# Kernel optimization log

Measured on AMD Instinct MI355X. Metric: run time of the kernel, lower is better.

Reference implementation:

```python
import jax, jax.numpy as jnp
import numpy as np

V, D, H, F, L, M, T, B, MAXT = 32000, 1024, 16, 4096, 3, 1, 1024, 2, 2048
HD = D // H

def _ln(x, g, b, eps=1e-5):
    m = x.mean(-1, keepdims=True)
    v = ((x - m) ** 2).mean(-1, keepdims=True)
    return (x - m) * jax.lax.rsqrt(v + eps) * g + b

def _mha(x, Wq, bq, Wk, bk, Wv, bv, Wo, bo, mask):
    Bx, Tx, Dx = x.shape
    q = (x @ Wq.T + bq).reshape(Bx, Tx, H, HD)
    k = (x @ Wk.T + bk).reshape(Bx, Tx, H, HD)
    v = (x @ Wv.T + bv).reshape(Bx, Tx, H, HD)
    s = jnp.einsum('bqhd,bkhd->bhqk', q, k) / np.float32(np.sqrt(HD))
    s = jnp.where(mask[None, None], s, jnp.float32(-1e9))
    a = jax.nn.softmax(s, axis=-1)
    o = jnp.einsum('bhqk,bkhd->bqhd', a, v).reshape(Bx, Tx, Dx)
    return o @ Wo.T + bo

def setup_inputs() -> dict:
    key = jax.random.key(0)
    ks = iter(jax.random.split(key, 64))
    rn = lambda shape: jax.random.normal(next(ks), shape, jnp.float32) * 0.02
    inp = {
        'x': jax.random.randint(next(ks), (B, T), 0, V),
        'mask': jnp.tril(jnp.ones((T, T), bool)),  # causal mask
        'tok_W': rn((V, D)),  # embedding table = Linear(V,D).weight.T
        'pos_embed': rn((MAXT, D)),
        'Wq': rn((L, D, D)), 'bq': jnp.zeros((L, D)),
        'Wk': rn((L, D, D)), 'bk': jnp.zeros((L, D)),
        'Wv': rn((L, D, D)), 'bv': jnp.zeros((L, D)),
        'Wo': rn((L, D, D)), 'bo': jnp.zeros((L, D)),
        'ln1_g': jnp.ones((L, D)), 'ln1_b': jnp.zeros((L, D)),
        'W1': rn((L, F, D)), 'b1': jnp.zeros((L, F)),
        'W2': rn((L, D, F)), 'b2': jnp.zeros((L, D)),
        'ln2_g': jnp.ones((L, D)), 'ln2_b': jnp.zeros((L, D)),
        'mWq': rn((M, D, D)), 'mbq': jnp.zeros((M, D)),
        'mWk': rn((M, D, D)), 'mbk': jnp.zeros((M, D)),
        'mWv': rn((M, D, D)), 'mbv': jnp.zeros((M, D)),
        'mWo': rn((M, D, D)), 'mbo': jnp.zeros((M, D)),
        'mln_g': jnp.ones((M, D)), 'mln_b': jnp.zeros((M, D)),
        'tWq': rn((D, D)), 'tbq': jnp.zeros((D,)),
        'tWk': rn((D, D)), 'tbk': jnp.zeros((D,)),
        'tWv': rn((D, D)), 'tbv': jnp.zeros((D,)),
        'tWo': rn((D, D)), 'tbo': jnp.zeros((D,)),
        'tln_g': jnp.ones((D,)), 'tln_b': jnp.zeros((D,)),
        'norm_g': jnp.ones((D,)), 'norm_b': jnp.zeros((D,)),
        'out_W': rn((V, D)), 'out_b': jnp.zeros((V,)),
    }
    return inp

def reference(x, mask, tok_W, pos_embed, Wq, bq, Wk, bk, Wv, bv, Wo, bo,
              ln1_g, ln1_b, W1, b1, W2, b2, ln2_g, ln2_b,
              mWq, mbq, mWk, mbk, mWv, mbv, mWo, mbo, mln_g, mln_b,
              tWq, tbq, tWk, tbk, tWv, tbv, tWo, tbo, tln_g, tln_b,
              norm_g, norm_b, out_W, out_b):
    Bx, Tx = x.shape
    # one_hot(x, V).float() @ W_tok^T  ==  gather row x from the (V, D) table
    h = jnp.take(tok_W, x, axis=0) + pos_embed[:Tx][None]
    mi = 0
    for i in range(L):  # static small layer count
        a = _mha(h, Wq[i], bq[i], Wk[i], bk[i], Wv[i], bv[i], Wo[i], bo[i], mask)
        h = _ln(h + a, ln1_g[i], ln1_b[i])
        f = jax.nn.gelu(h @ W1[i].T + b1[i]) @ W2[i].T + b2[i]
        h = _ln(h + f, ln2_g[i], ln2_b[i])
        if i % 3 == 2 and mi < M:  # memory layer every 3rd block
            a = _mha(h, mWq[mi], mbq[mi], mWk[mi], mbk[mi], mWv[mi], mbv[mi], mWo[mi], mbo[mi], mask)
            h = _ln(h + a, mln_g[mi], mln_b[mi])
            mi += 1
    a = _mha(h, tWq, tbq, tWk, tbk, tWv, tbv, tWo, tbo, mask)  # thought attention
    h = _ln(h + a, tln_g, tln_b)
    h = _ln(h, norm_g, norm_b)
    return h @ out_W.T + out_b  # [B, T, V] logits
```

## Files before the change

kernel.cpp:

```cpp
#include <hip/hip_runtime.h>
#include <cstdint>

#define DEV static __device__ __forceinline__

typedef unsigned short u16;
typedef __attribute__((ext_vector_type(8))) short short8;
typedef __attribute__((ext_vector_type(4))) float f32x4;

namespace cfg {
constexpr int V = 32000, D = 1024, H = 16, F = 4096, L = 3, T = 1024, B = 2;
constexpr int N = B * T;
constexpr int HD = D / H;
}

DEV float bf2f(u16 b) { union { unsigned u; float f; } x; x.u = (unsigned)b << 16; return x.f; }
DEV u16 f2bf(float f) {
  union { float f; unsigned u; } x; x.f = f;
  unsigned u = x.u;
  return (u16)((u + 0x7fffu + ((u >> 16) & 1u)) >> 16);
}

DEV void gload16(void* lds, const void* g) {
  __builtin_amdgcn_global_load_lds((__attribute__((address_space(1))) void*)g,
                                   (__attribute__((address_space(3))) void*)lds, 16, 0, 0);
}

DEV float waveSum(float v) {
#pragma unroll
  for (int o = 32; o; o >>= 1) v += __shfl_xor(v, o);
  return v;
}

struct CastJob { const float* src; u16* dst; int nBlk; };
struct CastArgs { CastJob j[24]; int n; };

__global__ void cast_kernel(CastArgs a) {
  int blk = blockIdx.x;
  int i = 0;
  while (i + 1 < a.n && blk >= a.j[i].nBlk) { blk -= a.j[i].nBlk; ++i; }
  const size_t base = (size_t)blk * 2048 + threadIdx.x * 8;
  const float4* s4 = (const float4*)(a.j[i].src + base);
  const float4 v0 = s4[0], v1 = s4[1];
  short8 o;
  o[0] = (short)f2bf(v0.x); o[1] = (short)f2bf(v0.y);
  o[2] = (short)f2bf(v0.z); o[3] = (short)f2bf(v0.w);
  o[4] = (short)f2bf(v1.x); o[5] = (short)f2bf(v1.y);
  o[6] = (short)f2bf(v1.z); o[7] = (short)f2bf(v1.w);
  *(short8*)(a.j[i].dst + base) = o;
}

struct CopyJob { const float* src; float* dst; };
struct CopyArgs { CopyJob j[16]; int n; };
__global__ void bconcat_kernel(CopyArgs a) {
  const CopyJob jb = a.j[blockIdx.x];
  ((float4*)jb.dst)[threadIdx.x] = ((const float4*)jb.src)[threadIdx.x];
}

__global__ void embed_kernel(const int* __restrict__ x, const float* __restrict__ tokW,
                             const float* __restrict__ pos, float* __restrict__ hF,
                             u16* __restrict__ hB) {
  const int bt = blockIdx.x;
  const int t = bt & (cfg::T - 1);
  const int tid = threadIdx.x;
  const int idx = x[bt];
  float4 v = ((const float4*)(tokW + (size_t)idx * cfg::D))[tid];
  const float4 p = ((const float4*)(pos + (size_t)t * cfg::D))[tid];
  v.x += p.x; v.y += p.y; v.z += p.z; v.w += p.w;
  ((float4*)(hF + (size_t)bt * cfg::D))[tid] = v;
  union { u16 u[4]; uint2 q; } pk;
  pk.u[0] = f2bf(v.x); pk.u[1] = f2bf(v.y); pk.u[2] = f2bf(v.z); pk.u[3] = f2bf(v.w);
  *(uint2*)(hB + (size_t)bt * cfg::D + tid * 4) = pk.q;
}

__global__ void ln_kernel(const float* __restrict__ base, const float* __restrict__ add,
                          const float* __restrict__ g, const float* __restrict__ bt,
                          float* __restrict__ outF, u16* __restrict__ outB) {
  const int row = blockIdx.x, tid = threadIdx.x;
  const int lane = tid & 63, wid = tid >> 6;
  float4 x = ((const float4*)(base + (size_t)row * cfg::D))[tid];
  if (add) {
    const float4 a = ((const float4*)(add + (size_t)row * cfg::D))[tid];
    x.x += a.x; x.y += a.y; x.z += a.z; x.w += a.w;
  }
  float s = x.x + x.y + x.z + x.w;
  float s2 = x.x * x.x + x.y * x.y + x.z * x.z + x.w * x.w;
  __shared__ float sb[8];
  s = waveSum(s); s2 = waveSum(s2);
  if (lane == 0) { sb[wid] = s; sb[4 + wid] = s2; }
  __syncthreads();
  s = sb[0] + sb[1] + sb[2] + sb[3];
  s2 = sb[4] + sb[5] + sb[6] + sb[7];
  const float mean = s * (1.f / cfg::D);
  const float rs = rsqrtf(s2 * (1.f / cfg::D) - mean * mean + 1e-5f);
  const float4 gv = ((const float4*)g)[tid];
  const float4 bv = ((const float4*)bt)[tid];
  float4 y;
  y.x = (x.x - mean) * rs * gv.x + bv.x;
  y.y = (x.y - mean) * rs * gv.y + bv.y;
  y.z = (x.z - mean) * rs * gv.z + bv.z;
  y.w = (x.w - mean) * rs * gv.w + bv.w;
  ((float4*)(outF + (size_t)row * cfg::D))[tid] = y;
  union { u16 u[4]; uint2 q; } pk;
  pk.u[0] = f2bf(y.x); pk.u[1] = f2bf(y.y); pk.u[2] = f2bf(y.z); pk.u[3] = f2bf(y.w);
  *(uint2*)(outB + (size_t)row * cfg::D + tid * 4) = pk.q;
}

__global__ void vtrans_kernel(const u16* __restrict__ v, u16* __restrict__ vtO, int vstride) {
  __shared__ u16 s[64][68];
  const int bh = blockIdx.y, b = bh >> 4, h = bh & 15;
  const int t0 = blockIdx.x * 64;
  const int tid = threadIdx.x;
  const int r2 = tid >> 3, cg = tid & 7;
#pragma unroll
  for (int p = 0; p < 2; ++p) {
    const int r = p * 32 + r2;
    const short8 val = *(const short8*)(v + (size_t)(b * cfg::T + t0 + r) * vstride + h * 64 + cg * 8);
#pragma unroll
    for (int j = 0; j < 8; ++j) s[r][cg * 8 + j] = (u16)val[j];
  }
  __syncthreads();
#pragma unroll
  for (int p = 0; p < 2; ++p) {
    const int d = p * 32 + r2;
    short8 o;
#pragma unroll
    for (int j = 0; j < 8; ++j) o[j] = (short)s[cg * 8 + j][d];
    *(short8*)(vtO + ((size_t)bh * 64 + d) * (size_t)cfg::T + t0 + cg * 8) = o;
  }
}

template <int NCH>
DEV void stageTile(u16* lds, const u16* src, int strideElems, int tid) {
#pragma unroll
  for (int c = 0; c < NCH / 256; ++c) {
    const int ci = c * 256 + tid;
    const int r = ci >> 3;
    const int c8 = ci & 7;
    const int sc8 = c8 ^ (r & 7);
    gload16(lds + (size_t)ci * 8, src + (size_t)r * strideElems + sc8 * 8);
  }
}
DEV short8 ldsFrag(const u16* tile, int row, int kElem) {
  const int byteoff = row * 128 + ((kElem * 2) ^ ((row & 7) << 4));
  return *(const short8*)((const char*)tile + byteoff);
}

__launch_bounds__(256, 2)
__global__ void fattn_kernel(const u16* __restrict__ qkv, const u16* __restrict__ vt,
                             u16* __restrict__ o) {
  constexpr int D3 = 3 * cfg::D;
  __shared__ u16 Qs[64 * 64];
  __shared__ u16 Ks[64 * 64];
  __shared__ u16 Vs[64 * 64];
  __shared__ u16 Ps[64][72];
  const int tid = threadIdx.x, lane = tid & 63, w = tid >> 6;
  const int qt = blockIdx.x, bh = blockIdx.y;
  const int b = bh >> 4, h = bh & 15;
  const int q0 = qt * 64;
  const int l15 = lane & 15, lq = lane >> 4;

  stageTile<512>(Qs, qkv + (size_t)(b * cfg::T + q0) * D3 + h * 64, D3, tid);
  __syncthreads();
  short8 qf[2];
#pragma unroll
  for (int kk = 0; kk < 2; ++kk)
    qf[kk] = ldsFrag(Qs, w * 16 + l15, kk * 32 + lq * 8);

  f32x4 oa[4];
  float m[4], l[4];
#pragma unroll
  for (int r = 0; r < 4; ++r) { m[r] = -1e30f; l[r] = 0.f; }
#pragma unroll
  for (int nt = 0; nt < 4; ++nt) { oa[nt][0] = 0; oa[nt][1] = 0; oa[nt][2] = 0; oa[nt][3] = 0; }

  const int nkt = qt + 1;
  const u16* kbase = qkv + (size_t)(b * cfg::T) * D3 + cfg::D + h * 64;
  const u16* vbase = vt + (size_t)bh * 64 * cfg::T;

  for (int kt = 0; kt < nkt; ++kt) {
    const int k0 = kt * 64;
    __syncthreads();
    stageTile<512>(Ks, kbase + (size_t)k0 * D3, D3, tid);
    stageTile<512>(Vs, vbase + k0, cfg::T, tid);
    __syncthreads();

    f32x4 sa[4];
#pragma unroll
    for (int nt = 0; nt < 4; ++nt) { sa[nt][0] = 0; sa[nt][1] = 0; sa[nt][2] = 0; sa[nt][3] = 0; }
#pragma unroll
    for (int kk = 0; kk < 2; ++kk) {
      short8 kf[4];
#pragma unroll
      for (int nt = 0; nt < 4; ++nt) kf[nt] = ldsFrag(Ks, nt * 16 + l15, kk * 32 + lq * 8);
#pragma unroll
      for (int nt = 0; nt < 4; ++nt)
        sa[nt] = __builtin_amdgcn_mfma_f32_16x16x32_bf16(qf[kk], kf[nt], sa[nt], 0, 0, 0);
    }

    const bool needMask = (kt >= qt);
#pragma unroll
    for (int r = 0; r < 4; ++r) {
      const int qrow = q0 + w * 16 + lq * 4 + r;
      float s[4];
#pragma unroll
      for (int nt = 0; nt < 4; ++nt) {
        s[nt] = sa[nt][r] * 0.125f;
        if (needMask && (k0 + nt * 16 + l15 > qrow)) s[nt] = -3e38f;
      }
      float rm = fmaxf(fmaxf(s[0], s[1]), fmaxf(s[2], s[3]));
#pragma unroll
      for (int off = 1; off < 16; off <<= 1) rm = fmaxf(rm, __shfl_xor(rm, off));
      const float mn = fmaxf(m[r], rm);
      const float sc = __expf(m[r] - mn);
      m[r] = mn;
      float ps = 0.f;
#pragma unroll
      for (int nt = 0; nt < 4; ++nt) {
        const float p = __expf(s[nt] - mn);
        ps += p;
        Ps[w * 16 + lq * 4 + r][nt * 16 + l15] = f2bf(p);
      }
#pragma unroll
      for (int off = 1; off < 16; off <<= 1) ps += __shfl_xor(ps, off);
      l[r] = l[r] * sc + ps;
#pragma unroll
      for (int nt = 0; nt < 4; ++nt) oa[nt][r] *= sc;
    }

#pragma unroll
    for (int kk = 0; kk < 2; ++kk) {
      short8 pa = *(const short8*)&Ps[w * 16 + l15][kk * 32 + lq * 8];
      short8 vf[4];
#pragma unroll
      for (int nt = 0; nt < 4; ++nt) vf[nt] = ldsFrag(Vs, nt * 16 + l15, kk * 32 + lq * 8);
#pragma unroll
      for (int nt = 0; nt < 4; ++nt)
        oa[nt] = __builtin_amdgcn_mfma_f32_16x16x32_bf16(pa, vf[nt], oa[nt], 0, 0, 0);
    }
  }

  u16* obase = o + (size_t)(b * cfg::T + q0 + w * 16) * cfg::D + h * 64;
#pragma unroll
  for (int r = 0; r < 4; ++r) {
    const float inv = 1.f / l[r];
    const int rl = lq * 4 + r;
#pragma unroll
    for (int nt = 0; nt < 4; ++nt)
      obase[(size_t)rl * cfg::D + nt * 16 + l15] = f2bf(oa[nt][r] * inv);
  }
}

template <int BN, int EPI, int OUTF32, int SWZ, int MMAJOR>
__launch_bounds__(256, 4)
__global__ void gemm_kernel(const u16* __restrict__ A, const u16* __restrict__ Bw,
                            const float* __restrict__ bias, void* __restrict__ Cp,
                            int lda, int ldb, int ldc, int K) {
  constexpr int BM = 128, BK = 64;
  constexpr int WN = BN / 2;
  constexpr int MF = 4, NF = WN / 16;
  int bx = blockIdx.x, by = blockIdx.y;
  if (SWZ) {
    const int gx = gridDim.x;
    const int nwg = gx * gridDim.y;
    const int lid = by * gx + bx;
    const int q = nwg >> 3, r = nwg & 7;
    const int xcd = lid & 7, rest = lid >> 3;
    const int nid = (xcd < r ? xcd * (q + 1) : r * (q + 1) + (xcd - r) * q) + rest;
    bx = nid % gx; by = nid / gx;
  }
  const int tid = threadIdx.x;
  const int lane = tid & 63;
  const int wid = tid >> 6;
  const int wr = wid >> 1, wc = wid & 1;
  const int m0 = (MMAJOR ? bx : by) * BM;
  const int n0 = (MMAJOR ? by : bx) * BN;

  __shared__ u16 As[BM][BK];
  __shared__ u16 Bs[BN][BK];

  const int nkt = K / BK;

  f32x4 acc[MF][NF];
#pragma unroll
  for (int i = 0; i < MF; ++i)
#pragma unroll
    for (int j = 0; j < NF; ++j) {
      acc[i][j][0] = 0.f; acc[i][j][1] = 0.f; acc[i][j][2] = 0.f; acc[i][j][3] = 0.f;
    }

  for (int kt = 0; kt < nkt; ++kt) {
    __syncthreads();
    const int kb = kt * BK;
    stageTile<(BM * BK) / 8>(&As[0][0], A + (size_t)m0 * lda + kb, lda, tid);
    stageTile<(BN * BK) / 8>(&Bs[0][0], Bw + (size_t)n0 * ldb + kb, ldb, tid);
    __syncthreads();
#pragma unroll
    for (int kk = 0; kk < BK / 32; ++kk) {
      short8 av[MF], bv[NF];
      const int kElem = kk * 32 + (lane >> 4) * 8;
#pragma unroll
      for (int mt = 0; mt < MF; ++mt)
        av[mt] = ldsFrag(&As[0][0], wr * 64 + mt * 16 + (lane & 15), kElem);
#pragma unroll
      for (int nt = 0; nt < NF; ++nt)
        bv[nt] = ldsFrag(&Bs[0][0], wc * WN + nt * 16 + (lane & 15), kElem);
#pragma unroll
      for (int mt = 0; mt < MF; ++mt)
#pragma unroll
        for (int nt = 0; nt < NF; ++nt)
          acc[mt][nt] = __builtin_amdgcn_mfma_f32_16x16x32_bf16(av[mt], bv[nt], acc[mt][nt], 0, 0, 0);
    }
  }

  const int rhi = (lane >> 4) * 4, cidx = lane & 15;
#pragma unroll
  for (int mt = 0; mt < MF; ++mt) {
#pragma unroll
    for (int nt = 0; nt < NF; ++nt) {
      const int col = n0 + wc * WN + nt * 16 + cidx;
      const float badd = bias ? bias[col] : 0.f;
#pragma unroll
      for (int r = 0; r < 4; ++r) {
        const int row = m0 + wr * 64 + mt * 16 + rhi + r;
        float val = acc[mt][nt][r] + badd;
        if (EPI == 1) {
          const float zz = 1.5957691216057308f * (val + 0.044715f * val * val * val);
          const float th = 1.f - 2.f / (__expf(zz) + 1.f);
          val = 0.5f * val * (1.f + th);
        }
        const size_t off = (size_t)row * ldc + col;
        if (OUTF32) ((float*)Cp)[off] = val;
        else ((u16*)Cp)[off] = f2bf(val);
      }
    }
  }
}

extern "C" void kernel_launch(void* const* d_in, const int* in_sizes, int n_in,
                              void* d_out, int out_size, void* d_ws, size_t ws_size,
                              hipStream_t stream) {
  using namespace cfg;
  (void)in_sizes; (void)n_in; (void)out_size;
  const int* x = (const int*)d_in[0];
  const float* tokW = (const float*)d_in[2];
  const float* pos = (const float*)d_in[3];
  const float* Wq = (const float*)d_in[4];  const float* bq = (const float*)d_in[5];
  const float* Wk = (const float*)d_in[6];  const float* bk = (const float*)d_in[7];
  const float* Wv = (const float*)d_in[8];  const float* bv = (const float*)d_in[9];
  const float* Wo = (const float*)d_in[10]; const float* bo = (const float*)d_in[11];
  const float* ln1g = (const float*)d_in[12]; const float* ln1b = (const float*)d_in[13];
  const float* W1 = (const float*)d_in[14]; const float* b1 = (const float*)d_in[15];
  const float* W2 = (const float*)d_in[16]; const float* b2 = (const float*)d_in[17];
  const float* ln2g = (const float*)d_in[18]; const float* ln2b = (const float*)d_in[19];
  const float* mWq = (const float*)d_in[20]; const float* mbq = (const float*)d_in[21];
  const float* mWk = (const float*)d_in[22]; const float* mbk = (const float*)d_in[23];
  const float* mWv = (const float*)d_in[24]; const float* mbv = (const float*)d_in[25];
  const float* mWo = (const float*)d_in[26]; const float* mbo = (const float*)d_in[27];
  const float* mlng = (const float*)d_in[28]; const float* mlnb = (const float*)d_in[29];
  const float* tWq = (const float*)d_in[30]; const float* tbq = (const float*)d_in[31];
  const float* tWk = (const float*)d_in[32]; const float* tbk = (const float*)d_in[33];
  const float* tWv = (const float*)d_in[34]; const float* tbv = (const float*)d_in[35];
  const float* tWo = (const float*)d_in[36]; const float* tbo = (const float*)d_in[37];
  const float* tlng = (const float*)d_in[38]; const float* tlnb = (const float*)d_in[39];
  const float* normg = (const float*)d_in[40]; const float* normb = (const float*)d_in[41];
  const float* outW = (const float*)d_in[42]; const float* outb = (const float*)d_in[43];

  const size_t DD = (size_t)D * D;
  char* wsb = (char*)d_ws;
  size_t off = 0;
  auto alloc = [&](size_t bytes) {
    void* p = wsb + off;
    off += (bytes + 255) & ~(size_t)255;
    return p;
  };
  u16* qkvW = (u16*)alloc((size_t)L * 3 * DD * 2);
  u16* mqkvW = (u16*)alloc(3 * DD * 2);
  u16* tqkvW = (u16*)alloc(3 * DD * 2);
  u16* WoB = (u16*)alloc((size_t)L * DD * 2);
  u16* W1B = (u16*)alloc((size_t)L * F * D * 2);
  u16* W2B = (u16*)alloc((size_t)L * D * F * 2);
  u16* mWoB = (u16*)alloc(DD * 2);
  u16* tWoB = (u16*)alloc(DD * 2);
  u16* outWB = (u16*)alloc((size_t)V * D * 2);
  float* biasQKV = (float*)alloc((size_t)(L + 2) * 3 * D * 4);
  float* hF = (float*)alloc((size_t)N * D * 4);
  u16* hB = (u16*)alloc((size_t)N * D * 2);
  float* aF = (float*)alloc((size_t)N * D * 4);
  u16* qkvB = (u16*)alloc((size_t)N * 3 * D * 2);
  u16* vtB = (u16*)alloc((size_t)N * D * 2);
  u16* oB = (u16*)alloc((size_t)N * D * 2);
  u16* f1B = (u16*)alloc((size_t)N * F * 2);
  if (off > ws_size) return;

  CastArgs ca;
  int nj = 0; long total = 0;
  auto addJob = [&](const float* s, u16* dptr, size_t n) {
    ca.j[nj].src = s; ca.j[nj].dst = dptr; ca.j[nj].nBlk = (int)(n / 2048);
    total += (long)(n / 2048); ++nj;
  };
  for (int i = 0; i < L; ++i) {
    addJob(Wq + i * DD, qkvW + (size_t)i * 3 * DD, DD);
    addJob(Wk + i * DD, qkvW + (size_t)i * 3 * DD + DD, DD);
    addJob(Wv + i * DD, qkvW + (size_t)i * 3 * DD + 2 * DD, DD);
  }
  addJob(mWq, mqkvW, DD); addJob(mWk, mqkvW + DD, DD); addJob(mWv, mqkvW + 2 * DD, DD);
  addJob(tWq, tqkvW, DD); addJob(tWk, tqkvW + DD, DD); addJob(tWv, tqkvW + 2 * DD, DD);
  addJob(Wo, WoB, (size_t)L * DD);
  addJob(W1, W1B, (size_t)L * F * D);
  addJob(W2, W2B, (size_t)L * D * F);
  addJob(mWo, mWoB, DD); addJob(tWo, tWoB, DD);
  addJob(outW, outWB, (size_t)V * D);
  ca.n = nj;
  cast_kernel<<<dim3((unsigned)total), 256, 0, stream>>>(ca);

  CopyArgs cpa;
  int nc = 0;
  auto addCopy = [&](const float* s, float* dptr) { cpa.j[nc].src = s; cpa.j[nc].dst = dptr; ++nc; };
  for (int i = 0; i < L; ++i) {
    addCopy(bq + (size_t)i * D, biasQKV + (size_t)i * 3 * D);
    addCopy(bk + (size_t)i * D, biasQKV + (size_t)i * 3 * D + D);
    addCopy(bv + (size_t)i * D, biasQKV + (size_t)i * 3 * D + 2 * D);
  }
  addCopy(mbq, biasQKV + (size_t)L * 3 * D); addCopy(mbk, biasQKV + (size_t)L * 3 * D + D);
  addCopy(mbv, biasQKV + (size_t)L * 3 * D + 2 * D);
  addCopy(tbq, biasQKV + (size_t)(L + 1) * 3 * D); addCopy(tbk, biasQKV + (size_t)(L + 1) * 3 * D + D);
  addCopy(tbv, biasQKV + (size_t)(L + 1) * 3 * D + 2 * D);
  cpa.n = nc;
  bconcat_kernel<<<dim3((unsigned)nc), 256, 0, stream>>>(cpa);

  embed_kernel<<<N, 256, 0, stream>>>(x, tokW, pos, hF, hB);

  auto mha = [&](const u16* qkvw, const float* qkvbias, const u16* wo, const float* bo_) {
    gemm_kernel<64, 0, 0, 0, 0><<<dim3(3 * D / 64, N / 128, 1), 256, 0, stream>>>(
        hB, qkvw, qkvbias, qkvB, D, D, 3 * D, D);
    vtrans_kernel<<<dim3(T / 64, B * H), 256, 0, stream>>>(qkvB + 2 * D, vtB, 3 * D);
    fattn_kernel<<<dim3(T / 64, B * H), 256, 0, stream>>>(qkvB, vtB, oB);
    gemm_kernel<64, 0, 1, 0, 0><<<dim3(D / 64, N / 128, 1), 256, 0, stream>>>(
        oB, wo, bo_, aF, D, D, D, D);
  };

  auto lnK = [&](const float* addp, const float* g, const float* b_) {
    ln_kernel<<<N, 256, 0, stream>>>(hF, addp, g, b_, hF, hB);
  };

  int mi = 0;
  for (int i = 0; i < L; ++i) {
    mha(qkvW + (size_t)i * 3 * DD, biasQKV + (size_t)i * 3 * D,
        WoB + (size_t)i * DD, bo + (size_t)i * D);
    lnK(aF, ln1g + (size_t)i * D, ln1b + (size_t)i * D);
    gemm_kernel<64, 1, 0, 0, 0><<<dim3(F / 64, N / 128, 1), 256, 0, stream>>>(
        hB, W1B + (size_t)i * F * D, b1 + (size_t)i * F, f1B, D, D, F, D);
    gemm_kernel<64, 0, 1, 0, 0><<<dim3(D / 64, N / 128, 1), 256, 0, stream>>>(
        f1B, W2B + (size_t)i * D * F, b2 + (size_t)i * D, aF, F, F, D, F);
    lnK(aF, ln2g + (size_t)i * D, ln2b + (size_t)i * D);
    if (i % 3 == 2 && mi < 1) {
      mha(mqkvW, biasQKV + (size_t)L * 3 * D, mWoB, mbo);
      lnK(aF, mlng, mlnb);
      ++mi;
    }
  }
  mha(tqkvW, biasQKV + (size_t)(L + 1) * 3 * D, tWoB, tbo);
  lnK(aF, tlng, tlnb);
  lnK(nullptr, normg, normb);
  gemm_kernel<128, 0, 1, 1, 1><<<dim3(N / 128, V / 128, 1), 256, 0, stream>>>(
      hB, outWB, outb, (float*)d_out, D, D, V, D);
}
```

Before: 1.059 ms.

## Split-K the Wo and W2 GEMMs and reduce partials inside layernorm

Measured after the change: 940.2 us. 11.2% less time.

```diff
diff --git a/kernel.cpp b/kernel.cpp
--- a/kernel.cpp
+++ b/kernel.cpp
@@ -72,14 +72,35 @@
   *(uint2*)(hB + (size_t)bt * cfg::D + tid * 4) = pk.q;
 }
 
-__global__ void ln_kernel(const float* __restrict__ base, const float* __restrict__ add,
+template <int NADD>
+__global__ void ln_kernel(const float* __restrict__ base,
+                          const float* __restrict__ a0, const float* __restrict__ a1,
+                          const float* __restrict__ a2, const float* __restrict__ a3,
+                          const float* __restrict__ biasv,
                           const float* __restrict__ g, const float* __restrict__ bt,
                           float* __restrict__ outF, u16* __restrict__ outB) {
   const int row = blockIdx.x, tid = threadIdx.x;
   const int lane = tid & 63, wid = tid >> 6;
-  float4 x = ((const float4*)(base + (size_t)row * cfg::D))[tid];
-  if (add) {
-    const float4 a = ((const float4*)(add + (size_t)row * cfg::D))[tid];
+  const size_t roff = (size_t)row * cfg::D;
+  float4 x = ((const float4*)(base + roff))[tid];
+  if (NADD >= 1) {
+    const float4 a = ((const float4*)(a0 + roff))[tid];
+    x.x += a.x; x.y += a.y; x.z += a.z; x.w += a.w;
+  }
+  if (NADD >= 2) {
+    const float4 a = ((const float4*)(a1 + roff))[tid];
+    x.x += a.x; x.y += a.y; x.z += a.z; x.w += a.w;
+  }
+  if (NADD >= 3) {
+    const float4 a = ((const float4*)(a2 + roff))[tid];
+    x.x += a.x; x.y += a.y; x.z += a.z; x.w += a.w;
+  }
+  if (NADD >= 4) {
+    const float4 a = ((const float4*)(a3 + roff))[tid];
+    x.x += a.x; x.y += a.y; x.z += a.z; x.w += a.w;
+  }
+  if (biasv) {
+    const float4 a = ((const float4*)biasv)[tid];
     x.x += a.x; x.y += a.y; x.z += a.z; x.w += a.w;
   }
   float s = x.x + x.y + x.z + x.w;
@@ -99,10 +120,10 @@
   y.y = (x.y - mean) * rs * gv.y + bv.y;
   y.z = (x.z - mean) * rs * gv.z + bv.z;
   y.w = (x.w - mean) * rs * gv.w + bv.w;
-  ((float4*)(outF + (size_t)row * cfg::D))[tid] = y;
+  ((float4*)(outF + roff))[tid] = y;
   union { u16 u[4]; uint2 q; } pk;
   pk.u[0] = f2bf(y.x); pk.u[1] = f2bf(y.y); pk.u[2] = f2bf(y.z); pk.u[3] = f2bf(y.w);
-  *(uint2*)(outB + (size_t)row * cfg::D + tid * 4) = pk.q;
+  *(uint2*)(outB + roff + tid * 4) = pk.q;
 }
 
 __global__ void vtrans_kernel(const u16* __restrict__ v, u16* __restrict__ vtO, int vstride) {
@@ -254,7 +275,7 @@
 __launch_bounds__(256, 4)
 __global__ void gemm_kernel(const u16* __restrict__ A, const u16* __restrict__ Bw,
                             const float* __restrict__ bias, void* __restrict__ Cp,
-                            int lda, int ldb, int ldc, int K) {
+                            int lda, int ldb, int ldc, int K, long long partStride) {
   constexpr int BM = 128, BK = 64;
   constexpr int WN = BN / 2;
   constexpr int MF = 4, NF = WN / 16;
@@ -268,6 +289,9 @@
     const int nid = (xcd < r ? xcd * (q + 1) : r * (q + 1) + (xcd - r) * q) + rest;
     bx = nid % gx; by = nid / gx;
   }
+  const int z = blockIdx.z;
+  const u16* Ab = A + (size_t)z * K;
+  const u16* Bb = Bw + (size_t)z * K;
   const int tid = threadIdx.x;
   const int lane = tid & 63;
   const int wid = tid >> 6;
@@ -291,8 +315,8 @@
   for (int kt = 0; kt < nkt; ++kt) {
     __syncthreads();
     const int kb = kt * BK;
-    stageTile<(BM * BK) / 8>(&As[0][0], A + (size_t)m0 * lda + kb, lda, tid);
-    stageTile<(BN * BK) / 8>(&Bs[0][0], Bw + (size_t)n0 * ldb + kb, ldb, tid);
+    stageTile<(BM * BK) / 8>(&As[0][0], Ab + (size_t)m0 * lda + kb, lda, tid);
+    stageTile<(BN * BK) / 8>(&Bs[0][0], Bb + (size_t)n0 * ldb + kb, ldb, tid);
     __syncthreads();
 #pragma unroll
     for (int kk = 0; kk < BK / 32; ++kk) {
@@ -313,6 +337,7 @@
   }
 
   const int rhi = (lane >> 4) * 4, cidx = lane & 15;
+  const long long cb = (long long)z * partStride;
 #pragma unroll
   for (int mt = 0; mt < MF; ++mt) {
 #pragma unroll
@@ -328,7 +353,7 @@
           const float th = 1.f - 2.f / (__expf(zz) + 1.f);
           val = 0.5f * val * (1.f + th);
         }
-        const size_t off = (size_t)row * ldc + col;
+        const size_t off = (size_t)(cb + (long long)row * ldc + col);
         if (OUTF32) ((float*)Cp)[off] = val;
         else ((u16*)Cp)[off] = f2bf(val);
       }
@@ -366,6 +391,7 @@
   const float* outW = (const float*)d_in[42]; const float* outb = (const float*)d_in[43];
 
   const size_t DD = (size_t)D * D;
+  const long long ND = (long long)N * D;
   char* wsb = (char*)d_ws;
   size_t off = 0;
   auto alloc = [&](size_t bytes) {
@@ -385,7 +411,7 @@
   float* biasQKV = (float*)alloc((size_t)(L + 2) * 3 * D * 4);
   float* hF = (float*)alloc((size_t)N * D * 4);
   u16* hB = (u16*)alloc((size_t)N * D * 2);
-  float* aF = (float*)alloc((size_t)N * D * 4);
+  float* pS = (float*)alloc((size_t)4 * N * D * 4);
   u16* qkvB = (u16*)alloc((size_t)N * 3 * D * 2);
   u16* vtB = (u16*)alloc((size_t)N * D * 2);
   u16* oB = (u16*)alloc((size_t)N * D * 2);
@@ -430,38 +456,39 @@
 
   embed_kernel<<<N, 256, 0, stream>>>(x, tokW, pos, hF, hB);
 
-  auto mha = [&](const u16* qkvw, const float* qkvbias, const u16* wo, const float* bo_) {
+  auto mha = [&](const u16* qkvw, const float* qkvbias, const u16* wo) {
     gemm_kernel<64, 0, 0, 0, 0><<<dim3(3 * D / 64, N / 128, 1), 256, 0, stream>>>(
-        hB, qkvw, qkvbias, qkvB, D, D, 3 * D, D);
+        hB, qkvw, qkvbias, qkvB, D, D, 3 * D, D, 0);
     vtrans_kernel<<<dim3(T / 64, B * H), 256, 0, stream>>>(qkvB + 2 * D, vtB, 3 * D);
     fattn_kernel<<<dim3(T / 64, B * H), 256, 0, stream>>>(qkvB, vtB, oB);
-    gemm_kernel<64, 0, 1, 0, 0><<<dim3(D / 64, N / 128, 1), 256, 0, stream>>>(
-        oB, wo, bo_, aF, D, D, D, D);
+    gemm_kernel<64, 0, 1, 0, 0><<<dim3(D / 64, N / 128, 2), 256, 0, stream>>>(
+        oB, wo, nullptr, pS, D, D, D, 512, ND);
   };
-
-  auto lnK = [&](const float* addp, const float* g, const float* b_) {
-    ln_kernel<<<N, 256, 0, stream>>>(hF, addp, g, b_, hF, hB);
+  auto lnMha = [&](const float* obias, const float* g, const float* b_) {
+    ln_kernel<2><<<N, 256, 0, stream>>>(hF, pS, pS + ND, nullptr, nullptr, obias, g, b_, hF, hB);
   };
 
   int mi = 0;
   for (int i = 0; i < L; ++i) {
-    mha(qkvW + (size_t)i * 3 * DD, biasQKV + (size_t)i * 3 * D,
-        WoB + (size_t)i * DD, bo + (size_t)i * D);
-    lnK(aF, ln1g + (size_t)i * D, ln1b + (size_t)i * D);
+    mha(qkvW + (size_t)i * 3 * DD, biasQKV + (size_t)i * 3 * D, WoB + (size_t)i * DD);
+    lnMha(bo + (size_t)i * D, ln1g + (size_t)i * D, ln1b + (size_t)i * D);
     gemm_kernel<64, 1, 0, 0, 0><<<dim3(F / 64, N / 128, 1), 256, 0, stream>>>(
-        hB, W1B + (size_t)i * F * D, b1 + (size_t)i * F, f1B, D, D, F, D);
-    gemm_kernel<64, 0, 1, 0, 0><<<dim3(D / 64, N / 128, 1), 256, 0, stream>>>(
-        f1B, W2B + (size_t)i * D * F, b2 + (size_t)i * D, aF, F, F, D, F);
-    lnK(aF, ln2g + (size_t)i * D, ln2b + (size_t)i * D);
+        hB, W1B + (size_t)i * F * D, b1 + (size_t)i * F, f1B, D, D, F, D, 0);
+    gemm_kernel<64, 0, 1, 0, 0><<<dim3(D / 64, N / 128, 4), 256, 0, stream>>>(
+        f1B, W2B + (size_t)i * D * F, nullptr, pS, F, F, D, 1024, ND);
+    ln_kernel<4><<<N, 256, 0, stream>>>(hF, pS, pS + ND, pS + 2 * ND, pS + 3 * ND,
+                                        b2 + (size_t)i * D, ln2g + (size_t)i * D,
+                                        ln2b + (size_t)i * D, hF, hB);
     if (i % 3 == 2 && mi < 1) {
-      mha(mqkvW, biasQKV + (size_t)L * 3 * D, mWoB, mbo);
-      lnK(aF, mlng, mlnb);
+      mha(mqkvW, biasQKV + (size_t)L * 3 * D, mWoB);
+      lnMha(mbo, mlng, mlnb);
       ++mi;
     }
   }
-  mha(tqkvW, biasQKV + (size_t)(L + 1) * 3 * D, tWoB, tbo);
-  lnK(aF, tlng, tlnb);
-  lnK(nullptr, normg, normb);
+  mha(tqkvW, biasQKV + (size_t)(L + 1) * 3 * D, tWoB);
+  lnMha(tbo, tlng, tlnb);
+  ln_kernel<0><<<N, 256, 0, stream>>>(hF, nullptr, nullptr, nullptr, nullptr, nullptr,
+                                      normg, normb, hF, hB);
   gemm_kernel<128, 0, 1, 1, 1><<<dim3(N / 128, V / 128, 1), 256, 0, stream>>>(
-      hB, outWB, outb, (float*)d_out, D, D, V, D);
-}
+      hB, outWB, outb, (float*)d_out, D, D, V, D, 0);
+}
```
